# Kernel tuning notes

Hardware: AMD Instinct MI355X
Metric: run time of the kernel (lower is better)

## Reference

```python
import jax, jax.numpy as jnp
import numpy as np

# ---- static config (matches init_kwargs) ----
C = 256          # in_channels
NH = 8           # num_heads
DH = 32          # dim_head
INNER = NH * DH  # 256
WD, WH, WW = 4, 8, 8   # window_size
NW = WD * WH * WW      # tokens per window = 256
SCALE = DH ** -0.5
EPS = 1e-5


def _make_rel_index():
    # Swin-3D relative position index, shape (NW, NW), values in [0, (2Wd-1)(2Wh-1)(2Ww-1))
    coords = np.stack(np.meshgrid(np.arange(WD), np.arange(WH), np.arange(WW), indexing='ij'))
    cf = coords.reshape(3, -1)                      # (3, NW)
    rel = cf[:, :, None] - cf[:, None, :]           # (3, NW, NW)
    rel = rel.transpose(1, 2, 0).astype(np.int64)   # (NW, NW, 3)
    rel[..., 0] += WD - 1
    rel[..., 1] += WH - 1
    rel[..., 2] += WW - 1
    rel[..., 0] *= (2 * WH - 1) * (2 * WW - 1)
    rel[..., 1] *= (2 * WW - 1)
    return rel.sum(-1)                              # (NW, NW)


def setup_inputs() -> dict:
    key = jax.random.key(0)
    k = jax.random.split(key, 5)
    num_rel = (2 * WD - 1) * (2 * WH - 1) * (2 * WW - 1)  # 1575
    x = jax.random.normal(k[0], (1, C, 16, 64, 64), dtype=jnp.float32)
    return {
        'x': x,
        'ln_gamma': jnp.ones((C,), jnp.float32),
        'ln_beta': jnp.zeros((C,), jnp.float32),
        'w_qkv': jax.random.normal(k[1], (C, 3 * INNER), jnp.float32) * 0.02,
        'w_out': jax.random.normal(k[2], (INNER, C), jnp.float32) * 0.02,
        'b_out': jnp.zeros((C,), jnp.float32),
        'bias_table': jax.random.normal(k[3], (num_rel, NH), jnp.float32) * 0.02,
        'rel_index': jnp.asarray(_make_rel_index(), dtype=jnp.int32),
    }


def reference(x, ln_gamma, ln_beta, w_qkv, w_out, b_out, bias_table, rel_index):
    B, Cc, D, H, W = x.shape
    Gd, Gh, Gw = D // WD, H // WH, W // WW
    # --- window partition: (B,C,D,H,W) -> (B*Gd*Gh*Gw, NW, C) ---
    xw = x.reshape(B, Cc, Gd, WD, Gh, WH, Gw, WW)
    xw = xw.transpose(0, 2, 4, 6, 3, 5, 7, 1)           # B,Gd,Gh,Gw,Wd,Wh,Ww,C
    xw = xw.reshape(B * Gd * Gh * Gw, NW, Cc)
    # --- LayerNorm over channels ---
    mu = xw.mean(-1, keepdims=True)
    var = xw.var(-1, keepdims=True)
    xn = (xw - mu) * jax.lax.rsqrt(var + EPS) * ln_gamma + ln_beta
    # --- QKV projection (no bias) ---
    qkv = xn @ w_qkv                                     # (Bp, NW, 3*INNER)
    q, k_, v = jnp.split(qkv, 3, axis=-1)
    Bp = q.shape[0]
    q = q.reshape(Bp, NW, NH, DH)
    k_ = k_.reshape(Bp, NW, NH, DH)
    v = v.reshape(Bp, NW, NH, DH)
    # --- attention with relative position bias ---
    scores = jnp.einsum('bnhd,bmhd->bhnm', q, k_) * SCALE
    bias = bias_table[rel_index]                         # (NW, NW, NH)
    scores = scores + bias.transpose(2, 0, 1)[None]      # broadcast over windows
    attn = jax.nn.softmax(scores, axis=-1)
    out = jnp.einsum('bhnm,bmhd->bnhd', attn, v).reshape(Bp, NW, INNER)
    # --- output projection (dropout p=0 is identity) ---
    out = out @ w_out + b_out
    # --- merge windows back ---
    out = out.reshape(B, Gd, Gh, Gw, WD, WH, WW, Cc)
    out = out.transpose(0, 7, 1, 4, 2, 5, 3, 6).reshape(B, Cc, D, H, W)
    return out
```

## Files before the change

### kernel.cpp

```cpp
#include <hip/hip_runtime.h>
#include <hip/hip_bf16.h>

typedef __attribute__((ext_vector_type(8))) short short8;
typedef __attribute__((ext_vector_type(4))) short s16x4;
typedef __attribute__((ext_vector_type(4))) float f32x4;
typedef __attribute__((ext_vector_type(2))) unsigned int u32x2;

#define NWIN 256
#define NW   256
#define CH   256
#define NH   8
#define DH   32
#define QKV_LD 768
#define ATTN_SCALE 0.17677669529663687f
#define LOG2E 1.4426950408889634f
#define QSCALE (ATTN_SCALE * LOG2E)

__device__ __forceinline__ unsigned short f2bf(float f) {
  union { float f; unsigned u; } v; v.f = f;
  unsigned r = v.u + 0x7FFFu + ((v.u >> 16) & 1u);
  return (unsigned short)(r >> 16);
}
__device__ __forceinline__ float bf2f(unsigned short h) {
  union { unsigned u; float f; } v; v.u = ((unsigned)h) << 16;
  return v.f;
}
__device__ __forceinline__ int swz128(int row, int kb) { return row * 128 + (kb ^ ((row & 7) << 4)); }
__device__ __forceinline__ void gload16(const unsigned short* g, unsigned short* l) {
  __builtin_amdgcn_global_load_lds((const __attribute__((address_space(1))) unsigned int*)(g),
                                   (__attribute__((address_space(3))) unsigned int*)(l), 16, 0, 0);
}

__global__ __launch_bounds__(256) void k_prepw(const float* __restrict__ wqkv,
                                               const float* __restrict__ wout,
                                               unsigned short* __restrict__ wqh,
                                               unsigned short* __restrict__ wql,
                                               unsigned short* __restrict__ woh,
                                               unsigned short* __restrict__ wol) {
  int idx = blockIdx.x * 256 + threadIdx.x;
  {
    int k = idx / 768, n = idx % 768;
    float v = wqkv[idx];
    if (n < 256) v *= QSCALE;
    unsigned short hi = f2bf(v);
    wqh[n * 256 + k] = hi;
    wql[n * 256 + k] = f2bf(v - bf2f(hi));
  }
  if (idx < 65536) {
    int k = idx >> 8, n = idx & 255;
    float v = wout[idx];
    unsigned short hi = f2bf(v);
    woh[n * 256 + k] = hi;
    wol[n * 256 + k] = f2bf(v - bf2f(hi));
  }
}

__global__ __launch_bounds__(256) void k_prepbias(const float* __restrict__ table,
                                                  const int* __restrict__ relidx,
                                                  float* __restrict__ bias2) {
  int idx = blockIdx.x * 256 + threadIdx.x;
  int h = idx >> 16;
  int qk = idx & 65535;
  bias2[idx] = table[relidx[qk] * 8 + h] * LOG2E;
}

__global__ __launch_bounds__(256) void k_ln(const float* __restrict__ x,
                                            const float* __restrict__ gamma,
                                            const float* __restrict__ beta,
                                            unsigned short* __restrict__ xn) {
  __shared__ unsigned short buf[256][66];
  __shared__ float stats[2][4][64];
  int bid = blockIdx.x;
  int d = bid >> 6, h = bid & 63;
  int t = threadIdx.x;
  int w = t & 63, cq = t >> 6;
  const float* xrow = x + (size_t)d * 4096 + (size_t)h * 64;
  float s0 = 0.f, s1 = 0.f;
  for (int ci = 0; ci < 64; ++ci) {
    int c = ci * 4 + cq;
    float v = xrow[(size_t)c * 65536 + w];
    buf[c][w] = f2bf(v);
    s0 += v; s1 += v * v;
  }
  stats[0][cq][w] = s0; stats[1][cq][w] = s1;
  __syncthreads();
  int lane = t & 63, wv = t >> 6;
  int winb = (d >> 2) * 64 + (h >> 3) * 8;
  int tokb = (d & 3) * 64 + (h & 7) * 8;
  for (int wi = 0; wi < 16; ++wi) {
    int w2 = wi * 4 + wv;
    float sum = stats[0][0][w2] + stats[0][1][w2] + stats[0][2][w2] + stats[0][3][w2];
    float sq  = stats[1][0][w2] + stats[1][1][w2] + stats[1][2][w2] + stats[1][3][w2];
    float mu = sum * 0.00390625f;
    float var = sq * 0.00390625f - mu * mu;
    float rstd = rsqrtf(var + 1e-5f);
    int win = winb + (w2 >> 3);
    int tok = tokb + (w2 & 7);
    unsigned short* dst = xn + ((size_t)win * NW + tok) * CH;
    for (int cc = 0; cc < 4; ++cc) {
      int c = cc * 64 + lane;
      float v = bf2f(buf[c][w2]);
      dst[c] = f2bf((v - mu) * rstd * gamma[c] + beta[c]);
    }
  }
}

__global__ __launch_bounds__(256) void k_qkv(const unsigned short* __restrict__ xn,
                                             const unsigned short* __restrict__ bhi,
                                             const unsigned short* __restrict__ blo,
                                             unsigned short* __restrict__ qkv) {
  __shared__ unsigned short sA[8192], sBh[8192], sBl[8192];
  int t = threadIdx.x;
  int mbase = blockIdx.x << 7, nbase = blockIdx.y << 7;
  bool isV = nbase >= 512;
  int wid = t >> 6, lane = t & 63;
  int wm = wid >> 1, wn = wid & 1;
  f32x4 acc[4][4];
#pragma unroll
  for (int i = 0; i < 4; ++i)
#pragma unroll
    for (int j = 0; j < 4; ++j) acc[i][j] = (f32x4)(0.f);
  for (int kt = 0; kt < 4; ++kt) {
#pragma unroll
    for (int i = 0; i < 4; ++i) {
      int ch = t + (i << 8);
      int row = ch >> 3, s = ch & 7;
      int gs = s ^ (row & 7);
      size_t go = (size_t)(mbase + row) * 256 + (kt << 6) + (gs << 3);
      size_t gb = (size_t)(nbase + row) * 256 + (kt << 6) + (gs << 3);
      gload16(xn + go,  sA  + ch * 8);
      gload16(bhi + gb, sBh + ch * 8);
      if (isV) gload16(blo + gb, sBl + ch * 8);
    }
    __syncthreads();
#pragma unroll
    for (int kk = 0; kk < 2; ++kk) {
      int kb = (kk << 6) + ((lane >> 4) << 4);
      short8 a[4], bh[4], bl[4];
#pragma unroll
      for (int mi = 0; mi < 4; ++mi) {
        int row = (wm << 6) + (mi << 4) + (lane & 15);
        a[mi] = *(const short8*)((char*)sA + swz128(row, kb));
      }
#pragma unroll
      for (int ni = 0; ni < 4; ++ni) {
        int row = (wn << 6) + (ni << 4) + (lane & 15);
        bh[ni] = *(const short8*)((char*)sBh + swz128(row, kb));
        if (isV) bl[ni] = *(const short8*)((char*)sBl + swz128(row, kb));
      }
#pragma unroll
      for (int mi = 0; mi < 4; ++mi)
#pragma unroll
        for (int ni = 0; ni < 4; ++ni) {
          acc[mi][ni] = __builtin_amdgcn_mfma_f32_16x16x32_bf16(a[mi], bh[ni], acc[mi][ni], 0, 0, 0);
          if (isV)
            acc[mi][ni] = __builtin_amdgcn_mfma_f32_16x16x32_bf16(a[mi], bl[ni], acc[mi][ni], 0, 0, 0);
        }
    }
    __syncthreads();
  }
#pragma unroll
  for (int mi = 0; mi < 4; ++mi)
#pragma unroll
    for (int ni = 0; ni < 4; ++ni)
#pragma unroll
      for (int r = 0; r < 4; ++r) {
        int m = mbase + (wm << 6) + (mi << 4) + ((lane >> 4) << 2) + r;
        int n = nbase + (wn << 6) + (ni << 4) + (lane & 15);
        qkv[(size_t)m * QKV_LD + n] = f2bf(acc[mi][ni][r]);
      }
}

__global__ __launch_bounds__(256) void k_attn(const unsigned short* __restrict__ qkv,
                                              const float* __restrict__ bias2,
                                              unsigned short* __restrict__ attnout) {
  __shared__ unsigned short Vt[8192];
  __shared__ unsigned short Kt[8192];
  int win = blockIdx.x, head = blockIdx.y;
  int t = threadIdx.x, wid = t >> 6, lane = t & 63;
  int l15 = lane & 15, g = lane >> 4;
  const unsigned short* base = qkv + (size_t)win * NW * QKV_LD + head * DH;

  {
    const unsigned short* vrow = base + 2 * CH + (size_t)t * QKV_LD;
    short8 v0 = *(const short8*)(vrow);
    short8 v1 = *(const short8*)(vrow + 8);
    short8 v2 = *(const short8*)(vrow + 16);
    short8 v3 = *(const short8*)(vrow + 24);
    int tb = t * 2;
#pragma unroll
    for (int j = 0; j < 8; ++j) {
      int sj = tb ^ (j << 4);
      *(unsigned short*)((char*)Vt + (j)      * 512 + sj)       = (unsigned short)v0[j];
      *(unsigned short*)((char*)Vt + (8 + j)  * 512 + (sj ^ 8)) = (unsigned short)v1[j];
      *(unsigned short*)((char*)Vt + (16 + j) * 512 + sj)       = (unsigned short)v2[j];
      *(unsigned short*)((char*)Vt + (24 + j) * 512 + (sj ^ 8)) = (unsigned short)v3[j];
    }
  }
  {
    const unsigned short* krow = base + CH + (size_t)t * QKV_LD;
    short8 k0 = *(const short8*)(krow);
    short8 k1 = *(const short8*)(krow + 8);
    short8 k2 = *(const short8*)(krow + 16);
    short8 k3 = *(const short8*)(krow + 24);
    char* kd = (char*)Kt + t * 64;
    int ks = ((t >> 1) & 3) << 4;
    *(short8*)(kd + (0  ^ ks)) = k0;
    *(short8*)(kd + (16 ^ ks)) = k1;
    *(short8*)(kd + (32 ^ ks)) = k2;
    *(short8*)(kd + (48 ^ ks)) = k3;
  }
  short8 bq[4];
#pragma unroll
  for (int qt = 0; qt < 4; ++qt)
    bq[qt] = *(const short8*)(base + (size_t)(wid * 64 + qt * 16 + l15) * QKV_LD + g * 8);

  f32x4 o[4][2];
#pragma unroll
  for (int qt = 0; qt < 4; ++qt) { o[qt][0] = (f32x4)(0.f); o[qt][1] = (f32x4)(0.f); }
  float l_[4] = {0.f, 0.f, 0.f, 0.f};
  const f32x4 zero = (f32x4)(0.f);
  const float* bthread = bias2 + ((size_t)head << 16) + (size_t)(wid * 64 + l15) * 256 + g * 4;
  int vswz = ((l15 & 7) << 4) ^ (l15 & 8);
  int kswz = ((l15 >> 1) & 3) << 4;

  f32x4 nb0, nb1, nb2, nb3;
  {
    const float* bp = bthread;
    nb0 = *(const f32x4*)(bp);
    nb1 = *(const f32x4*)(bp + 16);
    nb2 = *(const f32x4*)(bp + 32);
    nb3 = *(const f32x4*)(bp + 48);
  }

  __syncthreads();

  for (int ck = 0; ck < 4; ++ck) {
    short8 ak[4];
#pragma unroll
    for (int tt = 0; tt < 4; ++tt)
      ak[tt] = *(const short8*)((char*)Kt + (ck * 64 + tt * 16 + l15) * 64 + ((g * 16) ^ kswz));
#pragma unroll
    for (int qt = 0; qt < 4; ++qt) {
      f32x4 cb[4];
      cb[0] = nb0; cb[1] = nb1; cb[2] = nb2; cb[3] = nb3;
      if (!(ck == 3 && qt == 3)) {
        int nqt = (qt + 1) & 3;
        int nck = (qt == 3) ? ck + 1 : ck;
        const float* bp = bthread + (size_t)nqt * 4096 + nck * 64;
        nb0 = *(const f32x4*)(bp);
        nb1 = *(const f32x4*)(bp + 16);
        nb2 = *(const f32x4*)(bp + 32);
        nb3 = *(const f32x4*)(bp + 48);
      }
      f32x4 z[4];
#pragma unroll
      for (int tt = 0; tt < 4; ++tt)
        z[tt] = __builtin_amdgcn_mfma_f32_16x16x32_bf16(ak[tt], bq[qt], zero, 0, 0, 0);
      u32x2 wPq[4];
#pragma unroll
      for (int tt = 0; tt < 4; ++tt) {
        float p0 = __builtin_amdgcn_exp2f(z[tt][0] + cb[tt][0]);
        float p1 = __builtin_amdgcn_exp2f(z[tt][1] + cb[tt][1]);
        float p2 = __builtin_amdgcn_exp2f(z[tt][2] + cb[tt][2]);
        float p3 = __builtin_amdgcn_exp2f(z[tt][3] + cb[tt][3]);
        l_[qt] += (p0 + p1) + (p2 + p3);
        __hip_bfloat162 lo = __float22bfloat162_rn(float2{p0, p1});
        __hip_bfloat162 hi = __float22bfloat162_rn(float2{p2, p3});
        u32x2 pk;
        pk.x = *(unsigned int*)&lo;
        pk.y = *(unsigned int*)&hi;
        wPq[tt] = pk;
      }
#pragma unroll
      for (int tt = 0; tt < 4; ++tt) {
        int tokb = (ck * 128 + tt * 32 + g * 8) ^ vswz;
#pragma unroll
        for (int dht = 0; dht < 2; ++dht) {
          s16x4 vb = *(const s16x4*)((char*)Vt + (dht * 16 + l15) * 512 + tokb);
          o[qt][dht] = __builtin_amdgcn_mfma_f32_16x16x16bf16_1k(
              __builtin_bit_cast(s16x4, wPq[tt]), vb, o[qt][dht], 0, 0, 0);
        }
      }
    }
  }
#pragma unroll
  for (int qt = 0; qt < 4; ++qt) {
    float lq = l_[qt];
    lq += __shfl_xor(lq, 16);
    lq += __shfl_xor(lq, 32);
    float linv = 1.0f / lq;
#pragma unroll
    for (int r = 0; r < 4; ++r) {
      float lr = __shfl(linv, g * 4 + r);
      int q = wid * 64 + qt * 16 + g * 4 + r;
      unsigned short* dst = attnout + ((size_t)(win * NW + q)) * CH + head * DH + l15;
      dst[0]  = f2bf(o[qt][0][r] * lr);
      dst[16] = f2bf(o[qt][1][r] * lr);
    }
  }
}

union SmemOP {
  struct { unsigned short A[8192], Bh[8192], Bl[8192]; } st;
  float ot[64][129];
};
__global__ __launch_bounds__(256) void k_outproj(const unsigned short* __restrict__ attnout,
                                                 const unsigned short* __restrict__ bhi,
                                                 const unsigned short* __restrict__ blo,
                                                 const float* __restrict__ bo,
                                                 float* __restrict__ out) {
  __shared__ SmemOP sm;
  int t = threadIdx.x;
  int mbase = blockIdx.x << 7, nbase = blockIdx.y << 7;
  int wid = t >> 6, lane = t & 63;
  int wm = wid >> 1, wn = wid & 1;
  f32x4 acc[4][4];
#pragma unroll
  for (int i = 0; i < 4; ++i)
#pragma unroll
    for (int j = 0; j < 4; ++j) acc[i][j] = (f32x4)(0.f);
  for (int kt = 0; kt < 4; ++kt) {
#pragma unroll
    for (int i = 0; i < 4; ++i) {
      int ch = t + (i << 8);
      int row = ch >> 3, c16 = ch & 7;
      size_t go = (size_t)(mbase + row) * 256 + (kt << 6) + (c16 << 3);
      short8 va = *(const short8*)(attnout + go);
      *(short8*)((char*)sm.st.A + swz128(row, c16 << 4)) = va;
      size_t gb = (size_t)(nbase + row) * 256 + (kt << 6) + (c16 << 3);
      short8 vh = *(const short8*)(bhi + gb);
      *(short8*)((char*)sm.st.Bh + swz128(row, c16 << 4)) = vh;
      short8 vl = *(const short8*)(blo + gb);
      *(short8*)((char*)sm.st.Bl + swz128(row, c16 << 4)) = vl;
    }
    __syncthreads();
#pragma unroll
    for (int kk = 0; kk < 2; ++kk) {
      int kb = (kk << 6) + ((lane >> 4) << 4);
      short8 a[4], bh[4], bl[4];
#pragma unroll
      for (int mi = 0; mi < 4; ++mi) {
        int row = (wm << 6) + (mi << 4) + (lane & 15);
        a[mi] = *(const short8*)((char*)sm.st.A + swz128(row, kb));
      }
#pragma unroll
      for (int ni = 0; ni < 4; ++ni) {
        int row = (wn << 6) + (ni << 4) + (lane & 15);
        bh[ni] = *(const short8*)((char*)sm.st.Bh + swz128(row, kb));
        bl[ni] = *(const short8*)((char*)sm.st.Bl + swz128(row, kb));
      }
#pragma unroll
      for (int mi = 0; mi < 4; ++mi)
#pragma unroll
        for (int ni = 0; ni < 4; ++ni) {
          acc[mi][ni] = __builtin_amdgcn_mfma_f32_16x16x32_bf16(a[mi], bh[ni], acc[mi][ni], 0, 0, 0);
          acc[mi][ni] = __builtin_amdgcn_mfma_f32_16x16x32_bf16(a[mi], bl[ni], acc[mi][ni], 0, 0, 0);
        }
    }
    __syncthreads();
  }
  int win = mbase >> 8;
  int tokbase = mbase & 255;
  int gd = win >> 6, gh = (win >> 3) & 7, gw = win & 7;
  size_t posw = (size_t)gd * 4 * 4096 + (size_t)gh * 8 * 64 + (size_t)gw * 8;
  for (int half = 0; half < 2; ++half) {
    if (wm == half) {
#pragma unroll
      for (int mi = 0; mi < 4; ++mi)
#pragma unroll
        for (int ni = 0; ni < 4; ++ni)
#pragma unroll
          for (int r = 0; r < 4; ++r)
            sm.ot[(mi << 4) + ((lane >> 4) << 2) + r][(wn << 6) + (ni << 4) + (lane & 15)] = acc[mi][ni][r];
    }
    __syncthreads();
    int tok = tokbase + half * 64 + lane;
    int td = tok >> 6, th = (tok >> 3) & 7, tw = tok & 7;
    size_t pos = posw + (size_t)td * 4096 + (size_t)th * 64 + tw;
    for (int cc = 0; cc < 32; ++cc) {
      int c = (cc << 2) + wid;
      float v = sm.ot[lane][c] + bo[nbase + c];
      out[(size_t)(nbase + c) * 65536 + pos] = v;
    }
    __syncthreads();
  }
}

extern "C" void kernel_launch(void* const* d_in, const int* in_sizes, int n_in,
                              void* d_out, int out_size, void* d_ws, size_t ws_size,
                              hipStream_t stream) {
  const float* x     = (const float*)d_in[0];
  const float* gamma = (const float*)d_in[1];
  const float* beta  = (const float*)d_in[2];
  const float* wqkv  = (const float*)d_in[3];
  const float* wout  = (const float*)d_in[4];
  const float* bout  = (const float*)d_in[5];
  const float* btab  = (const float*)d_in[6];
  const int*   ridx  = (const int*)d_in[7];
  float* out = (float*)d_out;
  char* ws = (char*)d_ws;
  unsigned short* xn   = (unsigned short*)(ws);
  unsigned short* qkv  = (unsigned short*)(ws + 33554432);
  unsigned short* wqh  = (unsigned short*)(ws + 134217728);
  unsigned short* wql  = (unsigned short*)(ws + 134610944);
  unsigned short* woh  = (unsigned short*)(ws + 135004160);
  unsigned short* wol  = (unsigned short*)(ws + 135135232);
  float* bias2         = (float*)(ws + 135266304);
  unsigned short* attnout = xn;

  k_prepw<<<dim3(768), dim3(256), 0, stream>>>(wqkv, wout, wqh, wql, woh, wol);
  k_prepbias<<<dim3(2048), dim3(256), 0, stream>>>(btab, ridx, bias2);
  k_ln<<<dim3(1024), dim3(256), 0, stream>>>(x, gamma, beta, xn);
  k_qkv<<<dim3(512, 6), dim3(256), 0, stream>>>(xn, wqh, wql, qkv);
  k_attn<<<dim3(256, 8), dim3(256), 0, stream>>>(qkv, bias2, attnout);
  k_outproj<<<dim3(512, 2), dim3(256), 0, stream>>>(attnout, woh, wol, bout, out);
}
```

Before: 216.9 us.

## Vectorize LN loads, store QKV head-major, add MFMA priority hints in attention

The LayerNorm kernel now loads four contiguous floats per thread, packs them into bf16 pairs, and keeps 16 partial stat slots per token instead of 4. The QKV GEMM writes its output in a head-major layout (matrix, head, token, dim), so each attention block reads contiguous 64-byte rows for Q, K and V instead of strided 768-element rows. The attention loop also raises wave priority around its MFMA sections with s_setprio. The scattered 2-byte stores in the QKV epilogue may cost more write efficiency than the attention side gains.

```diff
diff --git a/kernel.cpp b/kernel.cpp
--- a/kernel.cpp
+++ b/kernel.cpp
@@ -69,28 +69,35 @@
                                             const float* __restrict__ beta,
                                             unsigned short* __restrict__ xn) {
   __shared__ unsigned short buf[256][66];
-  __shared__ float stats[2][4][64];
+  __shared__ float stats[2][16][64];
   int bid = blockIdx.x;
   int d = bid >> 6, h = bid & 63;
   int t = threadIdx.x;
-  int w = t & 63, cq = t >> 6;
+  int wq = (t & 15) << 2;
+  int cp = t >> 4;
   const float* xrow = x + (size_t)d * 4096 + (size_t)h * 64;
-  float s0 = 0.f, s1 = 0.f;
-  for (int ci = 0; ci < 64; ++ci) {
-    int c = ci * 4 + cq;
-    float v = xrow[(size_t)c * 65536 + w];
-    buf[c][w] = f2bf(v);
-    s0 += v; s1 += v * v;
-  }
-  stats[0][cq][w] = s0; stats[1][cq][w] = s1;
+  float s0[4] = {0.f, 0.f, 0.f, 0.f}, s1[4] = {0.f, 0.f, 0.f, 0.f};
+  for (int ci = 0; ci < 16; ++ci) {
+    int c = ci * 16 + cp;
+    f32x4 v = *(const f32x4*)(xrow + (size_t)c * 65536 + wq);
+    unsigned pk01 = (unsigned)f2bf(v[0]) | ((unsigned)f2bf(v[1]) << 16);
+    unsigned pk23 = (unsigned)f2bf(v[2]) | ((unsigned)f2bf(v[3]) << 16);
+    *(unsigned*)&buf[c][wq]     = pk01;
+    *(unsigned*)&buf[c][wq + 2] = pk23;
+#pragma unroll
+    for (int j = 0; j < 4; ++j) { s0[j] += v[j]; s1[j] += v[j] * v[j]; }
+  }
+#pragma unroll
+  for (int j = 0; j < 4; ++j) { stats[0][cp][wq + j] = s0[j]; stats[1][cp][wq + j] = s1[j]; }
   __syncthreads();
   int lane = t & 63, wv = t >> 6;
   int winb = (d >> 2) * 64 + (h >> 3) * 8;
   int tokb = (d & 3) * 64 + (h & 7) * 8;
   for (int wi = 0; wi < 16; ++wi) {
     int w2 = wi * 4 + wv;
-    float sum = stats[0][0][w2] + stats[0][1][w2] + stats[0][2][w2] + stats[0][3][w2];
-    float sq  = stats[1][0][w2] + stats[1][1][w2] + stats[1][2][w2] + stats[1][3][w2];
+    float sum = 0.f, sq = 0.f;
+#pragma unroll
+    for (int i = 0; i < 16; ++i) { sum += stats[0][i][w2]; sq += stats[1][i][w2]; }
     float mu = sum * 0.00390625f;
     float var = sq * 0.00390625f - mu * mu;
     float rstd = rsqrtf(var + 1e-5f);
@@ -108,7 +115,7 @@
 __global__ __launch_bounds__(256) void k_qkv(const unsigned short* __restrict__ xn,
                                              const unsigned short* __restrict__ bhi,
                                              const unsigned short* __restrict__ blo,
-                                             unsigned short* __restrict__ qkv) {
+                                             unsigned short* __restrict__ qkvH) {
   __shared__ unsigned short sA[8192], sBh[8192], sBl[8192];
   int t = threadIdx.x;
   int mbase = blockIdx.x << 7, nbase = blockIdx.y << 7;
@@ -167,11 +174,12 @@
       for (int r = 0; r < 4; ++r) {
         int m = mbase + (wm << 6) + (mi << 4) + ((lane >> 4) << 2) + r;
         int n = nbase + (wn << 6) + (ni << 4) + (lane & 15);
-        qkv[(size_t)m * QKV_LD + n] = f2bf(acc[mi][ni][r]);
-      }
-}
-
-__global__ __launch_bounds__(256) void k_attn(const unsigned short* __restrict__ qkv,
+        int mat = n >> 8, hd = (n >> 5) & 7, dh = n & 31;
+        qkvH[((size_t)(mat * 8 + hd) * 65536 + m) * 32 + dh] = f2bf(acc[mi][ni][r]);
+      }
+}
+
+__global__ __launch_bounds__(256) void k_attn(const unsigned short* __restrict__ qkvH,
                                               const float* __restrict__ bias2,
                                               unsigned short* __restrict__ attnout) {
   __shared__ unsigned short Vt[8192];
@@ -179,10 +187,12 @@
   int win = blockIdx.x, head = blockIdx.y;
   int t = threadIdx.x, wid = t >> 6, lane = t & 63;
   int l15 = lane & 15, g = lane >> 4;
-  const unsigned short* base = qkv + (size_t)win * NW * QKV_LD + head * DH;
+  const unsigned short* Qg = qkvH + ((size_t)(head)      * 65536 + win * 256) * 32;
+  const unsigned short* Kg = qkvH + ((size_t)(8 + head)  * 65536 + win * 256) * 32;
+  const unsigned short* Vg = qkvH + ((size_t)(16 + head) * 65536 + win * 256) * 32;
 
   {
-    const unsigned short* vrow = base + 2 * CH + (size_t)t * QKV_LD;
+    const unsigned short* vrow = Vg + (size_t)t * 32;
     short8 v0 = *(const short8*)(vrow);
     short8 v1 = *(const short8*)(vrow + 8);
     short8 v2 = *(const short8*)(vrow + 16);
@@ -198,7 +208,7 @@
     }
   }
   {
-    const unsigned short* krow = base + CH + (size_t)t * QKV_LD;
+    const unsigned short* krow = Kg + (size_t)t * 32;
     short8 k0 = *(const short8*)(krow);
     short8 k1 = *(const short8*)(krow + 8);
     short8 k2 = *(const short8*)(krow + 16);
@@ -213,7 +223,7 @@
   short8 bq[4];
 #pragma unroll
   for (int qt = 0; qt < 4; ++qt)
-    bq[qt] = *(const short8*)(base + (size_t)(wid * 64 + qt * 16 + l15) * QKV_LD + g * 8);
+    bq[qt] = *(const short8*)(Qg + (size_t)(wid * 64 + qt * 16 + l15) * 32 + g * 8);
 
   f32x4 o[4][2];
 #pragma unroll
@@ -254,9 +264,11 @@
         nb3 = *(const f32x4*)(bp + 48);
       }
       f32x4 z[4];
+      __builtin_amdgcn_s_setprio(1);
 #pragma unroll
       for (int tt = 0; tt < 4; ++tt)
         z[tt] = __builtin_amdgcn_mfma_f32_16x16x32_bf16(ak[tt], bq[qt], zero, 0, 0, 0);
+      __builtin_amdgcn_s_setprio(0);
       u32x2 wPq[4];
 #pragma unroll
       for (int tt = 0; tt < 4; ++tt) {
@@ -272,6 +284,7 @@
         pk.y = *(unsigned int*)&hi;
         wPq[tt] = pk;
       }
+      __builtin_amdgcn_s_setprio(1);
 #pragma unroll
       for (int tt = 0; tt < 4; ++tt) {
         int tokb = (ck * 128 + tt * 32 + g * 8) ^ vswz;
@@ -282,6 +295,7 @@
               __builtin_bit_cast(s16x4, wPq[tt]), vb, o[qt][dht], 0, 0, 0);
         }
       }
+      __builtin_amdgcn_s_setprio(0);
     }
   }
 #pragma unroll
```

Measured after the change: 212.1 us. 1.02x faster.
